# Optimization experiments

Measured on AMD Instinct MI355X. Metric: run time of the kernel, lower is better.

## Reference

```python
import jax, jax.numpy as jnp
import numpy as np

LEAK = 0.2
TEMP = 0.1          # CausalMask temperature
SPARSITY_W = 0.1
MI_W = 0.01
DAG_W = 1.0

def _leaky(x):
    return jax.nn.leaky_relu(x, LEAK)

def setup_inputs() -> dict:
    key = jax.random.key(0)
    B, F, S, H = 4096, 512, 32, 512
    H2, CH = H // 2, 64
    P = S * (S - 1) // 2  # 496 MI estimators
    ks = jax.random.split(key, 32)
    def w(k, shape, fan_in):
        return jax.random.normal(k, shape, jnp.float32) / np.sqrt(fan_in)
    return {
        'features': jax.random.normal(ks[0], (B, F), jnp.float32),
        'eps':      jax.random.normal(ks[1], (B, S), jnp.float32),
        'enc_w1': w(ks[2], (F, H), F),   'enc_b1': w(ks[3], (H,), H),
        'enc_w2': w(ks[4], (H, 2 * S), H), 'enc_b2': w(ks[5], (2 * S,), H) * 0.1,
        'log_weight': jax.random.normal(ks[6], (S, S), jnp.float32) * 0.5,
        'mech_w1': w(ks[7], (S, S, H2), S), 'mech_b1': w(ks[8], (S, H2), H2),
        'mech_w2': w(ks[9], (S, H2), H2),   'mech_b2': w(ks[10], (S,), H2),
        'dec_w1': w(ks[11], (S, H), S),  'dec_b1': w(ks[12], (H,), H),
        'dec_w2': w(ks[13], (H, F), H),  'dec_b2': w(ks[14], (F,), H),
        'mi_w1': w(ks[15], (P, 2, CH), 2),  'mi_b1': w(ks[16], (P, CH), CH),
        'mi_w2': w(ks[17], (P, CH, CH), CH), 'mi_b2': w(ks[18], (P, CH), CH),
        'mi_w3': w(ks[19], (P, CH), CH),     'mi_b3': w(ks[20], (P,), CH),
    }

def _forward(features, eps, enc_w1, enc_b1, enc_w2, enc_b2, log_weight,
             mech_w1, mech_b1, mech_w2, mech_b2, dec_w1, dec_b1, dec_w2, dec_b2,
             mi_w1, mi_b1, mi_w2, mi_b2, mi_w3, mi_b3):
    S = log_weight.shape[0]
    # ---- encode ----
    h = _leaky(features @ enc_w1 + enc_b1)
    params = h @ enc_w2 + enc_b2
    mean, log_std = jnp.split(params, 2, axis=-1)
    std = jnp.exp(log_std)
    z = mean + std * eps                                   # [B,S]
    # ---- soft causal adjacency (training mode) ----
    eye = jnp.eye(S, dtype=features.dtype)
    upper = jnp.triu(jnp.ones((S, S), features.dtype), k=1)
    lw = log_weight * upper - 10.0 * eye
    A = jax.nn.sigmoid(lw / TEMP)                          # [S,S]
    # ---- apply_causal_structure: stoch_dim tiny MLPs, vectorized ----
    # z_parents[b,i,s] = z[b,s] * A[s,i]
    zp = z[:, None, :] * A.T[None, :, :]                   # [B,S,S]
    h1 = _leaky(jnp.einsum('bis,ish->bih', zp, mech_w1) + mech_b1)  # [B,S,H2]
    z_causal = jnp.einsum('bih,ih->bi', h1, mech_w2) + mech_b2      # [B,S]
    # ---- decode ----
    recon = _leaky(z_causal @ dec_w1 + dec_b1) @ dec_w2 + dec_b2    # [B,F]
    # ---- losses ----
    recon_loss = jnp.mean((recon - features) ** 2)
    kl_loss = 0.5 * jnp.sum(mean ** 2 + std ** 2 - 2.0 * log_std - 1.0, axis=-1).mean()
    Asig = jax.nn.sigmoid(log_weight)
    sparsity_loss = jnp.sum(jnp.abs(Asig))
    # MI: one tiny MLP per (i<j) pair, row-major order == torch loop order
    iu, ju = jnp.triu_indices(S, k=1)
    pair = jnp.stack([z[:, iu], z[:, ju]], axis=-1)        # [B,P,2]
    m1 = _leaky(jnp.einsum('bpi,pih->bph', pair, mi_w1) + mi_b1)
    m2 = _leaky(jnp.einsum('bph,phk->bpk', m1, mi_w2) + mi_b2)
    mi_est = (jnp.einsum('bph,ph->bp', m2, mi_w3) + mi_b3).mean(0)  # [P]
    mi_loss = jnp.sum(jax.nn.sigmoid(log_weight[iu, ju]) * mi_est)
    # DAG: truncated matrix-exponential trace penalty
    A2 = Asig * Asig
    expm = eye
    mp = eye
    fact = 1.0
    for i in range(1, 10):
        fact *= i
        mp = mp @ A2
        expm = expm + mp / fact
    dag_loss = (jnp.trace(expm) - S) ** 2
    total_loss = recon_loss + kl_loss + SPARSITY_W * sparsity_loss + MI_W * mi_loss + DAG_W * dag_loss
    return z_causal, mean, std, recon, total_loss, recon_loss, kl_loss, sparsity_loss, mi_loss, dag_loss

def reference(features, eps, enc_w1, enc_b1, enc_w2, enc_b2, log_weight,
              mech_w1, mech_b1, mech_w2, mech_b2, dec_w1, dec_b1, dec_w2, dec_b2,
              mi_w1, mi_b1, mi_w2, mi_b2, mi_w3, mi_b3):
    return _forward(features, eps, enc_w1, enc_b1, enc_w2, enc_b2, log_weight,
                    mech_w1, mech_b1, mech_w2, mech_b2, dec_w1, dec_b1, dec_w2, dec_b2,
                    mi_w1, mi_b1, mi_w2, mi_b2, mi_w3, mi_b3)
```

## Files before the change

### kernel.cpp

```cpp
#include <hip/hip_runtime.h>
#include <hip/hip_bf16.h>

typedef float f32x4 __attribute__((ext_vector_type(4)));
typedef float f32x2 __attribute__((ext_vector_type(2)));
typedef short s16x8 __attribute__((ext_vector_type(8)));

__device__ __forceinline__ float leaky2(float x){ return fmaf(0.4f, fabsf(x), 0.6f * x); }

__device__ __forceinline__ short f2bf(float f){
    return __builtin_bit_cast(short, __float2bfloat16(f));
}

__global__ __launch_bounds__(256) void k_cvt(
    const float* __restrict__ ew1,
    const float* __restrict__ ew2, const float* __restrict__ dw2,
    const float* __restrict__ mw1, const float* __restrict__ mw2,
    const float* __restrict__ dw1,
    short* __restrict__ w1p,
    short* __restrict__ ew2p, short* __restrict__ dw2p,
    short* __restrict__ mw1p, short* __restrict__ mw2p,
    short* __restrict__ dw1p,
    const float* __restrict__ lw, float* __restrict__ A,
    float* __restrict__ acc)
{
    if (blockIdx.x >= 2048){
        __shared__ float A2s[1024], mp[1024], red[256];
        const int t = threadIdx.x;
        float part = 0.f;
        #pragma unroll
        for (int q = 0; q < 4; ++q){
            int e = t * 4 + q;
            int r = e >> 5, c = e & 31;
            float v = lw[e];
            float sig = 1.f / (1.f + expf(-v));
            float l2 = (r < c) ? v * 10.f : ((r == c) ? -100.f : 0.f);
            A[e] = 1.f / (1.f + expf(-l2));
            part += sig;
            float a2 = sig * sig;
            A2s[e] = a2; mp[e] = a2;
        }
        red[t] = part; __syncthreads();
        for (int s = 128; s > 0; s >>= 1){ if (t < s) red[t] += red[t + s]; __syncthreads(); }
        if (t == 0) acc[2] = red[0];

        const float invf[10] = {0.f, 1.f, 0.5f, 1.6666667e-1f, 4.1666667e-2f,
                                8.3333333e-3f, 1.3888889e-3f, 1.9841270e-4f,
                                2.4801587e-5f, 2.7557319e-6f};
        float tr = 0.f;
        const int r = t >> 3, c0 = (t & 7) * 4;
        for (int n = 1; n <= 9; ++n){
            __syncthreads();
            if (t == 0){
                float s = 0.f;
                for (int k2 = 0; k2 < 32; ++k2) s += mp[k2 * 33];
                tr += s * invf[n];
            }
            if (n == 9) break;
            float av[4] = {0.f, 0.f, 0.f, 0.f};
            for (int k2 = 0; k2 < 32; ++k2){
                float m = mp[r * 32 + k2];
                #pragma unroll
                for (int q = 0; q < 4; ++q) av[q] = fmaf(m, A2s[k2 * 32 + c0 + q], av[q]);
            }
            __syncthreads();
            #pragma unroll
            for (int q = 0; q < 4; ++q) mp[r * 32 + c0 + q] = av[q];
        }
        if (t == 0) acc[3] = tr * tr;
        return;
    }
    for (int idx = blockIdx.x * 256 + threadIdx.x; idx < 2867200; idx += 2048 * 256){
        int s = idx;
        if (s < 262144){
            int k = s >> 9, n = s & 511;
            int lane = (((k >> 3) & 3) << 4) | (n & 15);
            w1p[((n >> 4) * 16 + (k >> 5)) * 512 + lane * 8 + (k & 7)] = f2bf(ew1[s]);
            continue;
        }
        s -= 262144;
        if (s < 32768){
            int k = s >> 6, n = s & 63;
            int lane = (((k >> 3) & 3) << 4) | (n & 15);
            ew2p[((n >> 4) * 16 + (k >> 5)) * 512 + lane * 8 + (k & 7)] = f2bf(ew2[s]);
            continue;
        }
        s -= 32768;
        if (s < 262144){
            int k = s >> 9, n = s & 511;
            int lane = (((k >> 3) & 3) << 4) | (n & 15);
            dw2p[((n >> 4) * 16 + (k >> 5)) * 512 + lane * 8 + (k & 7)] = f2bf(dw2[s]);
            continue;
        }
        s -= 262144;
        if (s < 262144){
            int i = s >> 13, r2 = s & 8191;
            int k = r2 >> 8, n = r2 & 255;
            int lane = (((k >> 3) & 3) << 4) | (n & 15);
            mw1p[i * 8192 + (n >> 4) * 512 + lane * 8 + (k & 7)] = f2bf(mw1[s]);
            continue;
        }
        s -= 262144;
        if (s < 2031616){
            int p = s >> 12, r2 = s & 4095;
            int k = r2 >> 6, n = r2 & 63;
            int lane = (((k >> 3) & 3) << 4) | (n & 15);
            mw2p[p * 4096 + ((n >> 4) * 2 + (k >> 5)) * 512 + lane * 8 + (k & 7)] = f2bf(mw2[s]);
            continue;
        }
        s -= 2031616;
        int k = s >> 9, n = s & 511;
        int lane = (((k >> 3) & 3) << 4) | (n & 15);
        dw1p[(n >> 4) * 512 + lane * 8 + (k & 7)] = f2bf(dw1[s]);
    }
}

__global__ __launch_bounds__(256) void k_encf(
    const float* __restrict__ feat, const short* __restrict__ w1p,
    const float* __restrict__ eb1, const short* __restrict__ ew2p,
    const float* __restrict__ eb2, const float* __restrict__ eps,
    float* __restrict__ omean, float* __restrict__ ostd,
    float* __restrict__ zt, float* __restrict__ accg)
{
    __shared__ short hlds[8192];
    __shared__ float P[16][65];
    __shared__ float zs[16][33];
    __shared__ float red[256];
    const int t = threadIdx.x, lane = t & 63, wv = t >> 6;
    const int ml = lane & 15, kg = lane >> 4;
    const int b0 = blockIdx.x * 16;

    f32x4 acc1[8] = {};
    for (int kt = 0; kt < 16; ++kt){
        const float* ap = &feat[(size_t)(b0 + ml) * 512 + kt * 32 + kg * 8];
        f32x4 a0 = *(const f32x4*)ap;
        f32x4 a1 = *(const f32x4*)(ap + 4);
        s16x8 a;
        #pragma unroll
        for (int e = 0; e < 4; ++e){
            a[e]     = f2bf(a0[e]);
            a[e + 4] = f2bf(a1[e]);
        }
        #pragma unroll
        for (int nf = 0; nf < 8; ++nf){
            s16x8 b = *(const s16x8*)&w1p[((wv * 8 + nf) * 16 + kt) * 512 + lane * 8];
            acc1[nf] = __builtin_amdgcn_mfma_f32_16x16x32_bf16(a, b, acc1[nf], 0, 0, 0);
        }
    }
    #pragma unroll
    for (int nf = 0; nf < 8; ++nf){
        int col = wv * 128 + nf * 16 + ml;
        float bv = eb1[col];
        #pragma unroll
        for (int r = 0; r < 4; ++r){
            int row = kg * 4 + r;
            int byte = (row * 1024 + col * 2) ^ ((row & 7) << 4);
            hlds[byte >> 1] = f2bf(leaky2(acc1[nf][r] + bv));
        }
    }
    __syncthreads();

    f32x4 acc2 = {};
    for (int kt = 0; kt < 16; ++kt){
        int byte = (ml * 1024 + kt * 64 + kg * 16) ^ ((ml & 7) << 4);
        s16x8 a = *(const s16x8*)((const char*)hlds + byte);
        s16x8 b = *(const s16x8*)&ew2p[(wv * 16 + kt) * 512 + lane * 8];
        acc2 = __builtin_amdgcn_mfma_f32_16x16x32_bf16(a, b, acc2, 0, 0, 0);
    }
    {
        int col = wv * 16 + ml;
        float bv = eb2[col];
        #pragma unroll
        for (int r = 0; r < 4; ++r)
            P[kg * 4 + r][col] = acc2[r] + bv;
    }
    __syncthreads();
    float klp = 0.f;
    #pragma unroll
    for (int q = 0; q < 2; ++q){
        int e = q * 256 + t;
        int row = e >> 5, n = e & 31;
        float mean = P[row][n], ls = P[row][n + 32];
        float sd = expf(ls);
        size_t o = (size_t)(b0 + row) * 32 + n;
        float z = fmaf(sd, eps[o], mean);
        omean[o] = mean; ostd[o] = sd;
        zs[row][n] = z;
        klp += mean * mean + sd * sd - 2.f * ls - 1.f;
    }
    __syncthreads();
    #pragma unroll
    for (int q = 0; q < 2; ++q){
        int e = q * 256 + t;
        int n = e >> 4, row = e & 15;
        zt[(size_t)n * 4096 + b0 + row] = zs[row][n];
    }
    red[t] = klp; __syncthreads();
    for (int s = 128; s > 0; s >>= 1){ if (t < s) red[t] += red[t + s]; __syncthreads(); }
    if (t == 0) atomicAdd(accg + 0, red[0]);
}

__global__ __launch_bounds__(256) void k_mimech(
    const float* __restrict__ zt,
    const float* __restrict__ w1g, const float* __restrict__ b1g,
    const short* __restrict__ w2p, const float* __restrict__ b2g,
    const float* __restrict__ w3g, float* __restrict__ macc,
    const float* __restrict__ A, const short* __restrict__ W1p,
    const float* __restrict__ mb1, const float* __restrict__ mw2,
    const float* __restrict__ mb2, float* __restrict__ out_zc)
{
    __shared__ float sA[32], sB1[256], sW2[256];
    const int t = threadIdx.x, lane = t & 63, wv = t >> 6;
    const int ml = lane & 15, kg = lane >> 4;
    if (blockIdx.x < 1984){
        const int p = blockIdx.x >> 2, bq = blockIdx.x & 3;
        int pi = 0, rem = p;
        while (rem >= 31 - pi){ rem -= 31 - pi; ++pi; }
        const int pj = pi + 1 + rem;

        const int zrow = wv * 16 + ml;
        const float* zi_b = zt + (size_t)pi * 4096 + bq * 1024 + zrow;
        const float* zj_b = zt + (size_t)pj * 4096 + bq * 1024 + zrow;

        f32x2 w10v[2][4], w11v[2][4], b1v[2][4];
        #pragma unroll
        for (int ks = 0; ks < 2; ++ks)
            #pragma unroll
            for (int q = 0; q < 4; ++q){
                int h = ks * 32 + kg * 8 + q * 2;
                w10v[ks][q] = *(const f32x2*)&w1g[p * 128 + h] * 0.6f;
                w11v[ks][q] = *(const f32x2*)&w1g[p * 128 + 64 + h] * 0.6f;
                b1v[ks][q]  = *(const f32x2*)&b1g[p * 64 + h] * 0.6f;
            }
        s16x8 bfr[4][2];
        f32x4 b2c[4];
        #pragma unroll
        for (int nb = 0; nb < 4; ++nb){
            float bv = b2g[p * 64 + nb * 16 + ml];
            b2c[nb][0] = bv; b2c[nb][1] = bv; b2c[nb][2] = bv; b2c[nb][3] = bv;
            #pragma unroll
            for (int ks = 0; ks < 2; ++ks)
                bfr[nb][ks] = *(const s16x8*)&w2p[(size_t)p * 4096 + (nb * 2 + ks) * 512 + lane * 8];
        }
        const f32x2 c23 = {0.66666669f, 0.66666669f};
        float slin[4] = {0.f, 0.f, 0.f, 0.f}, sabs[4] = {0.f, 0.f, 0.f, 0.f};
        #pragma unroll 1
        for (int tile = 0; tile < 16; ++tile){
            float zi_c = zi_b[tile * 64], zj_c = zj_b[tile * 64];
            f32x2 zi2 = {zi_c, zi_c}, zj2 = {zj_c, zj_c};
            s16x8 af0, af1;
            #pragma unroll
            for (int q = 0; q < 4; ++q){
                f32x2 m0 = __builtin_elementwise_fma(zi2, w10v[0][q],
                           __builtin_elementwise_fma(zj2, w11v[0][q], b1v[0][q]));
                m0 = __builtin_elementwise_fma(c23, __builtin_elementwise_abs(m0), m0);
                af0[q * 2] = f2bf(m0[0]); af0[q * 2 + 1] = f2bf(m0[1]);
                f32x2 m1 = __builtin_elementwise_fma(zi2, w10v[1][q],
                           __builtin_elementwise_fma(zj2, w11v[1][q], b1v[1][q]));
                m1 = __builtin_elementwise_fma(c23, __builtin_elementwise_abs(m1), m1);
                af1[q * 2] = f2bf(m1[0]); af1[q * 2 + 1] = f2bf(m1[1]);
            }
            #pragma unroll
            for (int nb = 0; nb < 4; ++nb){
                f32x4 d = __builtin_amdgcn_mfma_f32_16x16x32_bf16(af0, bfr[nb][0], b2c[nb], 0, 0, 0);
                d = __builtin_amdgcn_mfma_f32_16x16x32_bf16(af1, bfr[nb][1], d, 0, 0, 0);
                #pragma unroll
                for (int r2 = 0; r2 < 4; ++r2){
                    slin[nb] += d[r2];
                    sabs[nb] += fabsf(d[r2]);
                }
            }
        }
        float s = 0.f;
        #pragma unroll
        for (int nb = 0; nb < 4; ++nb){
            float w3 = w3g[p * 64 + nb * 16 + ml];
            s = fmaf(0.6f * w3, slin[nb], fmaf(0.4f * w3, sabs[nb], s));
        }
        #pragma unroll
        for (int off = 32; off; off >>= 1) s += __shfl_xor(s, off);
        if (lane == 0) atomicAdd(&macc[p], s);
    } else {
        const int bx = blockIdx.x - 1984;
        const int i = bx & 31;
        const int b0 = (bx >> 5) * 64 + wv * 16;
        if (t < 32) sA[t] = A[t * 32 + i];
        sB1[t] = mb1[i * 256 + t];
        sW2[t] = mw2[i * 256 + t];
        __syncthreads();
        float zv[8];
        #pragma unroll
        for (int q = 0; q < 8; ++q)
            zv[q] = zt[(size_t)(kg * 8 + q) * 4096 + b0 + ml];
        s16x8 af;
        #pragma unroll
        for (int q = 0; q < 8; ++q)
            af[q] = f2bf(zv[q] * sA[kg * 8 + q]);
        float s[4] = {0.f, 0.f, 0.f, 0.f};
        #pragma unroll
        for (int nt = 0; nt < 16; ++nt){
            s16x8 bf = *(const s16x8*)&W1p[i * 8192 + nt * 512 + lane * 8];
            int col = nt * 16 + ml;
            float b1e = sB1[col], w2v = sW2[col];
            f32x4 d;
            d[0] = b1e; d[1] = b1e; d[2] = b1e; d[3] = b1e;
            d = __builtin_amdgcn_mfma_f32_16x16x32_bf16(af, bf, d, 0, 0, 0);
            float w2a = 0.6f * w2v, w2b = 0.4f * w2v;
            #pragma unroll
            for (int r = 0; r < 4; ++r)
                s[r] = fmaf(w2a, d[r], fmaf(w2b, fabsf(d[r]), s[r]));
        }
        #pragma unroll
        for (int off = 1; off < 16; off <<= 1)
            #pragma unroll
            for (int r = 0; r < 4; ++r) s[r] += __shfl_xor(s[r], off);
        if (ml == 0){
            float bb = mb2[i];
            #pragma unroll
            for (int r = 0; r < 4; ++r){
                int b = b0 + kg * 4 + r;
                out_zc[(size_t)b * 32 + i] = s[r] + bb;
            }
        }
    }
}

__global__ __launch_bounds__(256) void k_decf(
    const float* __restrict__ zc, const short* __restrict__ dw1p,
    const float* __restrict__ db1, const short* __restrict__ dw2p,
    const float* __restrict__ db2, const float* __restrict__ feat,
    float* __restrict__ recon, float* __restrict__ accg)
{
    __shared__ short dlds[16384];
    __shared__ float red[256];
    const int t = threadIdx.x, lane = t & 63, wv = t >> 6;
    const int ml = lane & 15, kg = lane >> 4;
    const int b0 = blockIdx.x * 32;
    const int c0 = blockIdx.y * 128;

    s16x8 af[2];
    #pragma unroll
    for (int m = 0; m < 2; ++m){
        int row = b0 + m * 16 + ml;
        f32x4 z0 = *(const f32x4*)&zc[(size_t)row * 32 + kg * 8];
        f32x4 z1 = *(const f32x4*)&zc[(size_t)row * 32 + kg * 8 + 4];
        #pragma unroll
        for (int e = 0; e < 4; ++e){
            af[m][e] = f2bf(z0[e]);
            af[m][e + 4] = f2bf(z1[e]);
        }
    }
    #pragma unroll
    for (int nf = 0; nf < 8; ++nf){
        int nt = wv * 8 + nf;
        s16x8 bf = *(const s16x8*)&dw1p[nt * 512 + lane * 8];
        int col = nt * 16 + ml;
        float b1e = db1[col];
        f32x4 c; c[0] = b1e; c[1] = b1e; c[2] = b1e; c[3] = b1e;
        #pragma unroll
        for (int m = 0; m < 2; ++m){
            f32x4 d = __builtin_amdgcn_mfma_f32_16x16x32_bf16(af[m], bf, c, 0, 0, 0);
            #pragma unroll
            for (int r = 0; r < 4; ++r){
                int row = m * 16 + kg * 4 + r;
                int byte = (row * 1024 + col * 2) ^ ((row & 7) << 4);
                dlds[byte >> 1] = f2bf(leaky2(d[r]));
            }
        }
    }
    __syncthreads();

    f32x4 acc[2][2] = {};
    for (int kt = 0; kt < 16; ++kt){
        s16x8 a[2];
        #pragma unroll
        for (int m = 0; m < 2; ++m){
            int row = m * 16 + ml;
            int byte = (row * 1024 + kt * 64 + kg * 16) ^ ((row & 7) << 4);
            a[m] = *(const s16x8*)((const char*)dlds + byte);
        }
        #pragma unroll
        for (int j = 0; j < 2; ++j){
            int nt = (c0 >> 4) + wv * 2 + j;
            s16x8 b = *(const s16x8*)&dw2p[(nt * 16 + kt) * 512 + lane * 8];
            #pragma unroll
            for (int m = 0; m < 2; ++m)
                acc[m][j] = __builtin_amdgcn_mfma_f32_16x16x32_bf16(a[m], b, acc[m][j], 0, 0, 0);
        }
    }
    float lsum = 0.f;
    #pragma unroll
    for (int j = 0; j < 2; ++j){
        int col = c0 + (wv * 2 + j) * 16 + ml;
        float bv = db2[col];
        #pragma unroll
        for (int m = 0; m < 2; ++m)
            #pragma unroll
            for (int r = 0; r < 4; ++r){
                int row = b0 + m * 16 + kg * 4 + r;
                float v = acc[m][j][r] + bv;
                float d = v - feat[(size_t)row * 512 + col];
                lsum = fmaf(d, d, lsum);
                recon[(size_t)row * 512 + col] = v;
            }
    }
    red[t] = lsum; __syncthreads();
    for (int s = 128; s > 0; s >>= 1){ if (t < s) red[t] += red[t + s]; __syncthreads(); }
    if (t == 0) atomicAdd(accg + 1, red[0]);
}

__global__ void k_final(const float* __restrict__ acc, const float* __restrict__ lw,
                        const float* __restrict__ b3, float* __restrict__ outs)
{
    __shared__ float red[512];
    int t = threadIdx.x;
    float c = 0.f;
    if (t < 496){
        int pi = 0, rem = t;
        while (rem >= 31 - pi){ rem -= 31 - pi; ++pi; }
        int pj = pi + 1 + rem;
        float est = acc[4 + t] * (1.f / 4096.f) + b3[t];
        float w = 1.f / (1.f + expf(-lw[pi * 32 + pj]));
        c = w * est;
    }
    red[t] = c; __syncthreads();
    for (int s = 256; s > 0; s >>= 1){ if (t < s) red[t] += red[t + s]; __syncthreads(); }
    if (t == 0){
        float mi    = red[0];
        float recon = acc[1] * (1.f / (4096.f * 512.f));
        float kl    = 0.5f * acc[0] * (1.f / 4096.f);
        float sp    = acc[2], dag = acc[3];
        outs[0] = recon + kl + 0.1f * sp + 0.01f * mi + dag;
        outs[1] = recon; outs[2] = kl; outs[3] = sp; outs[4] = mi; outs[5] = dag;
    }
}

extern "C" void kernel_launch(void* const* d_in, const int* in_sizes, int n_in,
                              void* d_out, int out_size, void* d_ws, size_t ws_size,
                              hipStream_t stream)
{
    const float* features = (const float*)d_in[0];
    const float* eps      = (const float*)d_in[1];
    const float* enc_w1   = (const float*)d_in[2];
    const float* enc_b1   = (const float*)d_in[3];
    const float* enc_w2   = (const float*)d_in[4];
    const float* enc_b2   = (const float*)d_in[5];
    const float* log_w    = (const float*)d_in[6];
    const float* mech_w1  = (const float*)d_in[7];
    const float* mech_b1  = (const float*)d_in[8];
    const float* mech_w2  = (const float*)d_in[9];
    const float* mech_b2  = (const float*)d_in[10];
    const float* dec_w1   = (const float*)d_in[11];
    const float* dec_b1   = (const float*)d_in[12];
    const float* dec_w2   = (const float*)d_in[13];
    const float* dec_b2   = (const float*)d_in[14];
    const float* mi_w1    = (const float*)d_in[15];
    const float* mi_b1    = (const float*)d_in[16];
    const float* mi_w2    = (const float*)d_in[17];
    const float* mi_b2    = (const float*)d_in[18];
    const float* mi_w3    = (const float*)d_in[19];
    const float* mi_b3    = (const float*)d_in[20];

    float* W      = (float*)d_ws;
    float* zt     = W;
    float* Abuf   = W + 262144;
    float* accums = W + 263168;
    short* w1p    = (short*)(W + 263680);
    short* ew2p   = (short*)(W + 394752);
    short* dw2p   = (short*)(W + 411136);
    short* mw1p   = (short*)(W + 542208);
    short* mw2p   = (short*)(W + 673280);
    short* dw1p   = (short*)(W + 1689088);
    float* out    = (float*)d_out;

    hipMemsetAsync(accums, 0, 512 * sizeof(float), stream);
    k_cvt<<<2049, 256, 0, stream>>>(enc_w1, enc_w2, dec_w2, mech_w1, mi_w2, dec_w1,
                                    w1p, ew2p, dw2p, mw1p, mw2p, dw1p,
                                    log_w, Abuf, accums);
    k_encf<<<256, 256, 0, stream>>>(features, w1p, enc_b1, ew2p, enc_b2, eps,
                                    out + 131072, out + 262144, zt, accums);
    k_mimech<<<4032, 256, 0, stream>>>(zt, mi_w1, mi_b1, mw2p, mi_b2, mi_w3, accums + 4,
                                       Abuf, mw1p, mech_b1, mech_w2, mech_b2, out);
    k_decf<<<dim3(128, 4), 256, 0, stream>>>(out, dw1p, dec_b1, dw2p, dec_b2, features,
                                             out + 393216, accums);
    k_final<<<1, 512, 0, stream>>>(accums, log_w, mi_b3, out + 2490368);
}
```

Measured before the change: 132.2 us.

## Split MI and mechanism kernels, convert MI second-layer weights in-register, unroll tiles

Stops pre-converting the large MI second-layer weight tensor to packed bf16 in the conversion kernel. The MI kernel now reads fp32 weights directly and converts them to bf16 fragments in registers. This removes a full extra write and read pass over about 2M elements. The fused MI/mechanism kernel is split into two separate launches, and the MI tile loop is unrolled by two to raise MFMA instruction-level parallelism. The trade-off is uncoalesced strided fp32 loads in each MI block and one extra kernel launch. The old k_mimech is left behind with meaningless dead stores.

New measurement: 137.7 us. 4.1% more time.

```diff
diff --git a/kernel.cpp b/kernel.cpp
--- a/kernel.cpp
+++ b/kernel.cpp
@@ -14,12 +14,10 @@
 __global__ __launch_bounds__(256) void k_cvt(
     const float* __restrict__ ew1,
     const float* __restrict__ ew2, const float* __restrict__ dw2,
-    const float* __restrict__ mw1, const float* __restrict__ mw2,
-    const float* __restrict__ dw1,
+    const float* __restrict__ mw1, const float* __restrict__ dw1,
     short* __restrict__ w1p,
     short* __restrict__ ew2p, short* __restrict__ dw2p,
-    short* __restrict__ mw1p, short* __restrict__ mw2p,
-    short* __restrict__ dw1p,
+    short* __restrict__ mw1p, short* __restrict__ dw1p,
     const float* __restrict__ lw, float* __restrict__ A,
     float* __restrict__ acc)
 {
@@ -69,7 +67,7 @@
         if (t == 0) acc[3] = tr * tr;
         return;
     }
-    for (int idx = blockIdx.x * 256 + threadIdx.x; idx < 2867200; idx += 2048 * 256){
+    for (int idx = blockIdx.x * 256 + threadIdx.x; idx < 835584; idx += 2048 * 256){
         int s = idx;
         if (s < 262144){
             int k = s >> 9, n = s & 511;
@@ -100,14 +98,6 @@
             continue;
         }
         s -= 262144;
-        if (s < 2031616){
-            int p = s >> 12, r2 = s & 4095;
-            int k = r2 >> 6, n = r2 & 63;
-            int lane = (((k >> 3) & 3) << 4) | (n & 15);
-            mw2p[p * 4096 + ((n >> 4) * 2 + (k >> 5)) * 512 + lane * 8 + (k & 7)] = f2bf(mw2[s]);
-            continue;
-        }
-        s -= 2031616;
         int k = s >> 9, n = s & 511;
         int lane = (((k >> 3) & 3) << 4) | (n & 15);
         dw1p[(n >> 4) * 512 + lane * 8 + (k & 7)] = f2bf(dw1[s]);
@@ -202,7 +192,7 @@
 __global__ __launch_bounds__(256) void k_mimech(
     const float* __restrict__ zt,
     const float* __restrict__ w1g, const float* __restrict__ b1g,
-    const short* __restrict__ w2p, const float* __restrict__ b2g,
+    const float* __restrict__ w2g, const float* __restrict__ b2g,
     const float* __restrict__ w3g, float* __restrict__ macc,
     const float* __restrict__ A, const short* __restrict__ W1p,
     const float* __restrict__ mb1, const float* __restrict__ mw2,
@@ -238,35 +228,55 @@
             float bv = b2g[p * 64 + nb * 16 + ml];
             b2c[nb][0] = bv; b2c[nb][1] = bv; b2c[nb][2] = bv; b2c[nb][3] = bv;
             #pragma unroll
-            for (int ks = 0; ks < 2; ++ks)
-                bfr[nb][ks] = *(const s16x8*)&w2p[(size_t)p * 4096 + (nb * 2 + ks) * 512 + lane * 8];
+            for (int ks = 0; ks < 2; ++ks){
+                const float* src = mw2 + (size_t)p * 4096 + (ks * 32 + kg * 8) * 64 + nb * 16 + ml;
+                s16x8 f;
+                #pragma unroll
+                for (int e = 0; e < 8; ++e) f[e] = f2bf(src[e * 64]);
+                bfr[nb][ks] = f;
+            }
         }
         const f32x2 c23 = {0.66666669f, 0.66666669f};
         float slin[4] = {0.f, 0.f, 0.f, 0.f}, sabs[4] = {0.f, 0.f, 0.f, 0.f};
         #pragma unroll 1
-        for (int tile = 0; tile < 16; ++tile){
-            float zi_c = zi_b[tile * 64], zj_c = zj_b[tile * 64];
-            f32x2 zi2 = {zi_c, zi_c}, zj2 = {zj_c, zj_c};
-            s16x8 af0, af1;
+        for (int tile = 0; tile < 16; tile += 2){
+            float ziA = zi_b[tile * 64],      zjA = zj_b[tile * 64];
+            float ziB = zi_b[tile * 64 + 64], zjB = zj_b[tile * 64 + 64];
+            f32x2 ziA2 = {ziA, ziA}, zjA2 = {zjA, zjA};
+            f32x2 ziB2 = {ziB, ziB}, zjB2 = {zjB, zjB};
+            s16x8 afA0, afA1, afB0, afB1;
             #pragma unroll
             for (int q = 0; q < 4; ++q){
-                f32x2 m0 = __builtin_elementwise_fma(zi2, w10v[0][q],
-                           __builtin_elementwise_fma(zj2, w11v[0][q], b1v[0][q]));
-                m0 = __builtin_elementwise_fma(c23, __builtin_elementwise_abs(m0), m0);
-                af0[q * 2] = f2bf(m0[0]); af0[q * 2 + 1] = f2bf(m0[1]);
-                f32x2 m1 = __builtin_elementwise_fma(zi2, w10v[1][q],
-                           __builtin_elementwise_fma(zj2, w11v[1][q], b1v[1][q]));
-                m1 = __builtin_elementwise_fma(c23, __builtin_elementwise_abs(m1), m1);
-                af1[q * 2] = f2bf(m1[0]); af1[q * 2 + 1] = f2bf(m1[1]);
+                f32x2 m;
+                m = __builtin_elementwise_fma(ziA2, w10v[0][q],
+                    __builtin_elementwise_fma(zjA2, w11v[0][q], b1v[0][q]));
+                m = __builtin_elementwise_fma(c23, __builtin_elementwise_abs(m), m);
+                afA0[q * 2] = f2bf(m[0]); afA0[q * 2 + 1] = f2bf(m[1]);
+                m = __builtin_elementwise_fma(ziA2, w10v[1][q],
+                    __builtin_elementwise_fma(zjA2, w11v[1][q], b1v[1][q]));
+                m = __builtin_elementwise_fma(c23, __builtin_elementwise_abs(m), m);
+                afA1[q * 2] = f2bf(m[0]); afA1[q * 2 + 1] = f2bf(m[1]);
+                m = __builtin_elementwise_fma(ziB2, w10v[0][q],
+                    __builtin_elementwise_fma(zjB2, w11v[0][q], b1v[0][q]));
+                m = __builtin_elementwise_fma(c23, __builtin_elementwise_abs(m), m);
+                afB0[q * 2] = f2bf(m[0]); afB0[q * 2 + 1] = f2bf(m[1]);
+                m = __builtin_elementwise_fma(ziB2, w10v[1][q],
+                    __builtin_elementwise_fma(zjB2, w11v[1][q], b1v[1][q]));
+                m = __builtin_elementwise_fma(c23, __builtin_elementwise_abs(m), m);
+                afB1[q * 2] = f2bf(m[0]); afB1[q * 2 + 1] = f2bf(m[1]);
             }
             #pragma unroll
             for (int nb = 0; nb < 4; ++nb){
-                f32x4 d = __builtin_amdgcn_mfma_f32_16x16x32_bf16(af0, bfr[nb][0], b2c[nb], 0, 0, 0);
-                d = __builtin_amdgcn_mfma_f32_16x16x32_bf16(af1, bfr[nb][1], d, 0, 0, 0);
+                f32x4 dA = __builtin_amdgcn_mfma_f32_16x16x32_bf16(afA0, bfr[nb][0], b2c[nb], 0, 0, 0);
+                dA = __builtin_amdgcn_mfma_f32_16x16x32_bf16(afA1, bfr[nb][1], dA, 0, 0, 0);
+                f32x4 dB = __builtin_amdgcn_mfma_f32_16x16x32_bf16(afB0, bfr[nb][0], b2c[nb], 0, 0, 0);
+                dB = __builtin_amdgcn_mfma_f32_16x16x32_bf16(afB1, bfr[nb][1], dB, 0, 0, 0);
                 #pragma unroll
                 for (int r2 = 0; r2 < 4; ++r2){
-                    slin[nb] += d[r2];
-                    sabs[nb] += fabsf(d[r2]);
+                    slin[nb] += dA[r2];
+                    sabs[nb] += fabsf(dA[r2]);
+                    slin[nb] += dB[r2];
+                    sabs[nb] += fabsf(dB[r2]);
                 }
             }
         }
@@ -285,9 +295,20 @@
         const int b0 = (bx >> 5) * 64 + wv * 16;
         if (t < 32) sA[t] = A[t * 32 + i];
         sB1[t] = mb1[i * 256 + t];
-        sW2[t] = mw2[i * 256 + t];
+        sW2[t] = mw2[0];
+        sW2[t] = mb1[i * 256 + t] * 0.f + ((const float*)A)[0] * 0.f;
         __syncthreads();
+        sW2[t] = 0.f;
+        __syncthreads();
+        sW2[t] = ((const float* __restrict__)mb2)[0] * 0.f;
+        __syncthreads();
+        sW2[t] = 0.f;
+        __syncthreads();
+        (void)0;
         float zv[8];
+        sW2[t] = 0.f; __syncthreads();
+        sW2[t] = ((const float*)W1p)[0] * 0.f;
+        __syncthreads();
         #pragma unroll
         for (int q = 0; q < 8; ++q)
             zv[q] = zt[(size_t)(kg * 8 + q) * 4096 + b0 + ml];
@@ -322,6 +343,154 @@
             }
         }
     }
+}
+
+__global__ __launch_bounds__(256) void k_mech(
+    const float* __restrict__ zt, const float* __restrict__ A,
+    const short* __restrict__ W1p, const float* __restrict__ mb1,
+    const float* __restrict__ mw2, const float* __restrict__ mb2,
+    float* __restrict__ out_zc)
+{
+    __shared__ float sA[32], sB1[256], sW2[256];
+    const int t = threadIdx.x, lane = t & 63, wv = t >> 6;
+    const int ml = lane & 15, kg = lane >> 4;
+    const int i = blockIdx.y;
+    const int b0 = blockIdx.x * 64 + wv * 16;
+    if (t < 32) sA[t] = A[t * 32 + i];
+    sB1[t] = mb1[i * 256 + t];
+    sW2[t] = mw2[i * 256 + t];
+    __syncthreads();
+    float zv[8];
+    #pragma unroll
+    for (int q = 0; q < 8; ++q)
+        zv[q] = zt[(size_t)(kg * 8 + q) * 4096 + b0 + ml];
+    s16x8 af;
+    #pragma unroll
+    for (int q = 0; q < 8; ++q)
+        af[q] = f2bf(zv[q] * sA[kg * 8 + q]);
+    float s[4] = {0.f, 0.f, 0.f, 0.f};
+    #pragma unroll
+    for (int nt = 0; nt < 16; ++nt){
+        s16x8 bf = *(const s16x8*)&W1p[i * 8192 + nt * 512 + lane * 8];
+        int col = nt * 16 + ml;
+        float b1e = sB1[col], w2v = sW2[col];
+        f32x4 d;
+        d[0] = b1e; d[1] = b1e; d[2] = b1e; d[3] = b1e;
+        d = __builtin_amdgcn_mfma_f32_16x16x32_bf16(af, bf, d, 0, 0, 0);
+        float w2a = 0.6f * w2v, w2b = 0.4f * w2v;
+        #pragma unroll
+        for (int r = 0; r < 4; ++r)
+            s[r] = fmaf(w2a, d[r], fmaf(w2b, fabsf(d[r]), s[r]));
+    }
+    #pragma unroll
+    for (int off = 1; off < 16; off <<= 1)
+        #pragma unroll
+        for (int r = 0; r < 4; ++r) s[r] += __shfl_xor(s[r], off);
+    if (ml == 0){
+        float bb = mb2[i];
+        #pragma unroll
+        for (int r = 0; r < 4; ++r){
+            int b = b0 + kg * 4 + r;
+            out_zc[(size_t)b * 32 + i] = s[r] + bb;
+        }
+    }
+}
+
+__global__ __launch_bounds__(256) void k_mi(
+    const float* __restrict__ zt,
+    const float* __restrict__ w1g, const float* __restrict__ b1g,
+    const float* __restrict__ w2g, const float* __restrict__ b2g,
+    const float* __restrict__ w3g, float* __restrict__ macc)
+{
+    const int t = threadIdx.x, lane = t & 63, wv = t >> 6;
+    const int ml = lane & 15, kg = lane >> 4;
+    const int p = blockIdx.x >> 2, bq = blockIdx.x & 3;
+    int pi = 0, rem = p;
+    while (rem >= 31 - pi){ rem -= 31 - pi; ++pi; }
+    const int pj = pi + 1 + rem;
+
+    const int zrow = wv * 16 + ml;
+    const float* zi_b = zt + (size_t)pi * 4096 + bq * 1024 + zrow;
+    const float* zj_b = zt + (size_t)pj * 4096 + bq * 1024 + zrow;
+
+    f32x2 w10v[2][4], w11v[2][4], b1v[2][4];
+    #pragma unroll
+    for (int ks = 0; ks < 2; ++ks)
+        #pragma unroll
+        for (int q = 0; q < 4; ++q){
+            int h = ks * 32 + kg * 8 + q * 2;
+            w10v[ks][q] = *(const f32x2*)&w1g[p * 128 + h] * 0.6f;
+            w11v[ks][q] = *(const f32x2*)&w1g[p * 128 + 64 + h] * 0.6f;
+            b1v[ks][q]  = *(const f32x2*)&b1g[p * 64 + h] * 0.6f;
+        }
+    s16x8 bfr[4][2];
+    f32x4 b2c[4];
+    #pragma unroll
+    for (int nb = 0; nb < 4; ++nb){
+        float bv = b2g[p * 64 + nb * 16 + ml];
+        b2c[nb][0] = bv; b2c[nb][1] = bv; b2c[nb][2] = bv; b2c[nb][3] = bv;
+        #pragma unroll
+        for (int ks = 0; ks < 2; ++ks){
+            const float* src = w2g + (size_t)p * 4096 + (ks * 32 + kg * 8) * 64 + nb * 16 + ml;
+            s16x8 f;
+            #pragma unroll
+            for (int e = 0; e < 8; ++e) f[e] = f2bf(src[e * 64]);
+            bfr[nb][ks] = f;
+        }
+    }
+    const f32x2 c23 = {0.66666669f, 0.66666669f};
+    float slin[4] = {0.f, 0.f, 0.f, 0.f}, sabs[4] = {0.f, 0.f, 0.f, 0.f};
+    #pragma unroll 1
+    for (int tile = 0; tile < 16; tile += 2){
+        float ziA = zi_b[tile * 64],      zjA = zj_b[tile * 64];
+        float ziB = zi_b[tile * 64 + 64], zjB = zj_b[tile * 64 + 64];
+        f32x2 ziA2 = {ziA, ziA}, zjA2 = {zjA, zjA};
+        f32x2 ziB2 = {ziB, ziB}, zjB2 = {zjB, zjB};
+        s16x8 afA0, afA1, afB0, afB1;
+        #pragma unroll
+        for (int q = 0; q < 4; ++q){
+            f32x2 m;
+            m = __builtin_elementwise_fma(ziA2, w10v[0][q],
+                __builtin_elementwise_fma(zjA2, w11v[0][q], b1v[0][q]));
+            m = __builtin_elementwise_fma(c23, __builtin_elementwise_abs(m), m);
+            afA0[q * 2] = f2bf(m[0]); afA0[q * 2 + 1] = f2bf(m[1]);
+            m = __builtin_elementwise_fma(ziA2, w10v[1][q],
+                __builtin_elementwise_fma(zjA2, w11v[1][q], b1v[1][q]));
+            m = __builtin_elementwise_fma(c23, __builtin_elementwise_abs(m), m);
+            afA1[q * 2] = f2bf(m[0]); afA1[q * 2 + 1] = f2bf(m[1]);
+            m = __builtin_elementwise_fma(ziB2, w10v[0][q],
+                __builtin_elementwise_fma(zjB2, w11v[0][q], b1v[0][q]));
+            m = __builtin_elementwise_fma(c23, __builtin_elementwise_abs(m), m);
+            afB0[q * 2] = f2bf(m[0]); afB0[q * 2 + 1] = f2bf(m[1]);
+            m = __builtin_elementwise_fma(ziB2, w10v[1][q],
+                __builtin_elementwise_fma(zjB2, w11v[1][q], b1v[1][q]));
+            m = __builtin_elementwise_fma(c23, __builtin_elementwise_abs(m), m);
+            afB1[q * 2] = f2bf(m[0]); afB1[q * 2 + 1] = f2bf(m[1]);
+        }
+        #pragma unroll
+        for (int nb = 0; nb < 4; ++nb){
+            f32x4 dA = __builtin_amdgcn_mfma_f32_16x16x32_bf16(afA0, bfr[nb][0], b2c[nb], 0, 0, 0);
+            dA = __builtin_amdgcn_mfma_f32_16x16x32_bf16(afA1, bfr[nb][1], dA, 0, 0, 0);
+            f32x4 dB = __builtin_amdgcn_mfma_f32_16x16x32_bf16(afB0, bfr[nb][0], b2c[nb], 0, 0, 0);
+            dB = __builtin_amdgcn_mfma_f32_16x16x32_bf16(afB1, bfr[nb][1], dB, 0, 0, 0);
+            #pragma unroll
+            for (int r2 = 0; r2 < 4; ++r2){
+                slin[nb] += dA[r2];
+                sabs[nb] += fabsf(dA[r2]);
+                slin[nb] += dB[r2];
+                sabs[nb] += fabsf(dB[r2]);
+            }
+        }
+    }
+    float s = 0.f;
+    #pragma unroll
+    for (int nb = 0; nb < 4; ++nb){
+        float w3 = w3g[p * 64 + nb * 16 + ml];
+        s = fmaf(0.6f * w3, slin[nb], fmaf(0.4f * w3, sabs[nb], s));
+    }
+    #pragma unroll
+    for (int off = 32; off; off >>= 1) s += __shfl_xor(s, off);
+    if (lane == 0) atomicAdd(&macc[p], s);
 }
 
 __global__ __launch_bounds__(256) void k_decf(
@@ -468,18 +637,17 @@
     short* ew2p   = (short*)(W + 394752);
     short* dw2p   = (short*)(W + 411136);
     short* mw1p   = (short*)(W + 542208);
-    short* mw2p   = (short*)(W + 673280);
-    short* dw1p   = (short*)(W + 1689088);
+    short* dw1p   = (short*)(W + 673280);
     float* out    = (float*)d_out;
 
     hipMemsetAsync(accums, 0, 512 * sizeof(float), stream);
-    k_cvt<<<2049, 256, 0, stream>>>(enc_w1, enc_w2, dec_w2, mech_w1, mi_w2, dec_w1,
-                                    w1p, ew2p, dw2p, mw1p, mw2p, dw1p,
+    k_cvt<<<2049, 256, 0, stream>>>(enc_w1, enc_w2, dec_w2, mech_w1, dec_w1,
+                                    w1p, ew2p, dw2p, mw1p, dw1p,
                                     log_w, Abuf, accums);
     k_encf<<<256, 256, 0, stream>>>(features, w1p, enc_b1, ew2p, enc_b2, eps,
                                     out + 131072, out + 262144, zt, accums);
-    k_mimech<<<4032, 256, 0, stream>>>(zt, mi_w1, mi_b1, mw2p, mi_b2, mi_w3, accums + 4,
-                                       Abuf, mw1p, mech_b1, mech_w2, mech_b2, out);
+    k_mi<<<1984, 256, 0, stream>>>(zt, mi_w1, mi_b1, mi_w2, mi_b2, mi_w3, accums + 4);
+    k_mech<<<dim3(64, 32), 256, 0, stream>>>(zt, Abuf, mw1p, mech_b1, mech_w2, mech_b2, out);
     k_decf<<<dim3(128, 4), 256, 0, stream>>>(out, dw1p, dec_b1, dw2p, dec_b2, features,
                                              out + 393216, accums);
     k_final<<<1, 512, 0, stream>>>(accums, log_w, mi_b3, out + 2490368);
```
